# Optimization experiments

Hardware: AMD Instinct MI355X
Metric: run time of the kernel (lower is better)

Reference implementation:

```python
import jax, jax.numpy as jnp
import numpy as np

N = 131072      # num nodes
T = 16          # tile (block) size, tile_rows == tile_cols
BR = N // T     # block rows = 8192
K = 8           # nonzero blocks per block-row
IN_F, HID, NCLS = 128, 256, 64
LN_EPS = 1e-5


def setup_inputs() -> dict:
    key = jax.random.key(0)
    ks = jax.random.split(key, 8)
    features = jax.random.normal(ks[0], (N, IN_F), dtype=jnp.float32)
    block_vals = jax.random.uniform(ks[1], (BR, K, T, T), dtype=jnp.float32) / (K * T)
    block_cols = jax.random.randint(ks[2], (BR, K), 0, BR, dtype=jnp.int32)
    W0 = jax.random.normal(ks[3], (IN_F, HID), dtype=jnp.float32) / np.sqrt(IN_F)
    W1 = jax.random.normal(ks[4], (HID, HID), dtype=jnp.float32) / np.sqrt(HID)
    W2 = jax.random.normal(ks[5], (HID, NCLS), dtype=jnp.float32) / np.sqrt(HID)
    return {
        "features": features,
        "block_vals": block_vals,
        "W0": W0, "b0": jnp.zeros((HID,), jnp.float32),
        "W1": W1, "b1": jnp.zeros((HID,), jnp.float32),
        "W2": W2, "b2": jnp.zeros((NCLS,), jnp.float32),
        "g0": jnp.ones((HID,), jnp.float32), "beta0": jnp.zeros((HID,), jnp.float32),
        "g1": jnp.ones((HID,), jnp.float32), "beta1": jnp.zeros((HID,), jnp.float32),
        "block_cols": block_cols,
    }


def bcsr_spmm(block_vals, block_cols, z):
    """Block-CSR sparse matmul: out = A @ z.
    block_vals: [BR, K, T, T], block_cols: [BR, K] (block-column ids), z: [N, F]."""
    f = z.shape[-1]
    zb = z.reshape(BR, T, f)[block_cols]          # gather column blocks -> [BR, K, T, F]
    out = jnp.einsum('bkrc,bkcf->brf', block_vals, zb)  # block GEMM + accumulate over K
    return out.reshape(N, f)


def layer_norm(x, g, b):
    mu = jnp.mean(x, axis=-1, keepdims=True)
    var = jnp.mean(jnp.square(x - mu), axis=-1, keepdims=True)
    return g * (x - mu) * jax.lax.rsqrt(var + LN_EPS) + b


def reference(features, block_vals, W0, b0, W1, b1, W2, b2,
              g0, beta0, g1, beta1, block_cols):
    # layer 0: h' = A @ (h W0) + b0 ; relu ; LayerNorm
    h = bcsr_spmm(block_vals, block_cols, features @ W0) + b0
    h = layer_norm(jax.nn.relu(h), g0, beta0)
    # layer 1
    h = bcsr_spmm(block_vals, block_cols, h @ W1) + b1
    h = layer_norm(jax.nn.relu(h), g1, beta1)
    # output layer (no activation/norm)
    h = bcsr_spmm(block_vals, block_cols, h @ W2) + b2
    return h
```

## Files before the change

### kernel.cpp

```cpp
#include <hip/hip_runtime.h>
#include <hip/hip_bf16.h>


typedef __bf16 bf16;
typedef bf16 bf16x8 __attribute__((ext_vector_type(8)));
typedef bf16 bf16x4 __attribute__((ext_vector_type(4)));
typedef float f32x4 __attribute__((ext_vector_type(4)));

#define N_NODES 131072
#define BRQ 8192
#define KNZ 8
#define IN_F 128
#define HID 256
#define NCLS 64

static __device__ __forceinline__ f32x4 mfma16(bf16x8 a, bf16x8 b, f32x4 c) {
  return __builtin_amdgcn_mfma_f32_16x16x32_bf16(a, b, c, 0, 0, 0);
}

static __device__ __forceinline__ bf16x8 load8(const bf16* p) {
  return *(const bf16x8*)p;
}
static __device__ __forceinline__ bf16x8 load8(const float* p) {
  f32x4 a0 = *(const f32x4*)p;
  f32x4 a1 = *(const f32x4*)(p + 4);
  bf16x8 r;
  r[0] = (bf16)a0[0]; r[1] = (bf16)a0[1]; r[2] = (bf16)a0[2]; r[3] = (bf16)a0[3];
  r[4] = (bf16)a1[0]; r[5] = (bf16)a1[1]; r[6] = (bf16)a1[2]; r[7] = (bf16)a1[3];
  return r;
}

__global__ void transpose_cvt(const float* __restrict__ in, bf16* __restrict__ out,
                              int rows, int cols) {
  int idx = blockIdx.x * 256 + threadIdx.x;
  if (idx < rows * cols) {
    int r = idx / cols, c = idx - r * cols;
    out[c * rows + r] = (bf16)in[idx];
  }
}

template<typename TA, int KIN, int FOUT, int GRID>
__global__ __launch_bounds__(256) void gemm_bt(const TA* __restrict__ X,
                                               const bf16* __restrict__ WT,
                                               bf16* __restrict__ Zbt) {
  constexpr int CG  = FOUT / 64;
  constexpr int KS  = KIN / 32;
  constexpr int RTS = GRID * 4 / CG;
  constexpr int NT  = BRQ / RTS;

  const int wave = threadIdx.x >> 6;
  const int lane = threadIdx.x & 63;
  const int l15  = lane & 15;
  const int quad = lane >> 4;
  const int gw   = blockIdx.x * 4 + wave;
  const int cg   = gw % CG;
  const int rt0  = gw / CG;

  const bf16* __restrict__ wbase = WT + (long)(cg * 64 + l15) * KIN + quad * 8;
  bf16x8 bfr[KS][4];
#pragma unroll
  for (int k = 0; k < KS; ++k)
#pragma unroll
    for (int t = 0; t < 4; ++t)
      bfr[k][t] = *(const bf16x8*)(wbase + t * (16 * KIN) + k * 32);

  const TA* __restrict__ xbase = X + (long)l15 * KIN + quad * 8;

  bf16x8 aw[2][KS];
#pragma unroll
  for (int k = 0; k < KS; ++k)
    aw[0][k] = load8(xbase + (long)rt0 * (16 * KIN) + k * 32);

#pragma unroll
  for (int it = 0; it < NT; ++it) {
    const int rt = rt0 + it * RTS;
    if (it + 1 < NT) {
      const long xoff = (long)(rt + RTS) * (16 * KIN);
#pragma unroll
      for (int k = 0; k < KS; ++k)
        aw[(it + 1) & 1][k] = load8(xbase + xoff + k * 32);
    }
    f32x4 acc[4] = {};
#pragma unroll
    for (int k = 0; k < KS; ++k)
#pragma unroll
      for (int t = 0; t < 4; ++t)
        acc[t] = mfma16(aw[it & 1][k], bfr[k][t], acc[t]);
#pragma unroll
    for (int t = 0; t < 4; ++t) {
      int col = cg * 64 + t * 16 + l15;
      bf16x4 v;
#pragma unroll
      for (int i = 0; i < 4; ++i) v[i] = (bf16)acc[t][i];
      *(bf16x4*)(Zbt + ((long)rt * FOUT + col) * 16 + quad * 4) = v;
    }
  }
}

__global__ __launch_bounds__(256) void spmm_ln(const float* __restrict__ Abv,
                                               const int*   __restrict__ Abc,
                                               const bf16*  __restrict__ Zbt,
                                               const float* __restrict__ bias,
                                               const float* __restrict__ gamma,
                                               const float* __restrict__ beta,
                                               bf16* __restrict__ H) {
  const int b    = blockIdx.x;
  const int wave = threadIdx.x >> 6;
  const int lane = threadIdx.x & 63;
  const int l15  = lane & 15;
  const int quad = lane >> 4;

  const int*   bc    = Abc + b * KNZ;
  const int    cst   = (quad & 1) * 8;
  const int    half  = quad >> 1;
  const float* abase = Abv + (long)b * (KNZ * 256) + l15 * 16 + cst;

  bf16x8 afr[4];
  long   zb[4];
#pragma unroll
  for (int kp = 0; kp < 4; ++kp) {
    int blk = 2 * kp + half;
    afr[kp] = load8(abase + blk * 256);
    zb[kp]  = (long)bc[blk] * (HID * 16) + cst;
  }
  bf16x8 bfr[4][4];
#pragma unroll
  for (int kp = 0; kp < 4; ++kp)
#pragma unroll
    for (int t = 0; t < 4; ++t) {
      int f = wave * 64 + t * 16 + l15;
      bfr[kp][t] = *(const bf16x8*)(Zbt + zb[kp] + f * 16);
    }

  f32x4 acc[4] = {};
#pragma unroll
  for (int kp = 0; kp < 4; ++kp)
#pragma unroll
    for (int t = 0; t < 4; ++t)
      acc[t] = mfma16(afr[kp], bfr[kp][t], acc[t]);

  __shared__ float ld[16][257];
#pragma unroll
  for (int t = 0; t < 4; ++t) {
    int f = wave * 64 + t * 16 + l15;
    float bi = bias[f];
#pragma unroll
    for (int i = 0; i < 4; ++i) {
      float v = acc[t][i] + bi;
      ld[quad * 4 + i][f] = v > 0.f ? v : 0.f;
    }
  }
  __syncthreads();

#pragma unroll
  for (int rr = 0; rr < 4; ++rr) {
    int r = wave * 4 + rr;
    float v0 = ld[r][lane], v1 = ld[r][64 + lane];
    float v2 = ld[r][128 + lane], v3 = ld[r][192 + lane];
    float s  = v0 + v1 + v2 + v3;
    float ss = v0 * v0 + v1 * v1 + v2 * v2 + v3 * v3;
#pragma unroll
    for (int m = 1; m < 64; m <<= 1) {
      s  += __shfl_xor(s, m, 64);
      ss += __shfl_xor(ss, m, 64);
    }
    float mu   = s * (1.f / 256.f);
    float var  = ss * (1.f / 256.f) - mu * mu;
    float rstd = rsqrtf(var + 1e-5f);
    bf16* hrow = H + (long)(b * 16 + r) * HID;
    float vv[4] = {v0, v1, v2, v3};
#pragma unroll
    for (int k2 = 0; k2 < 4; ++k2) {
      int f = k2 * 64 + lane;
      float y = (vv[k2] - mu) * rstd * gamma[f] + beta[f];
      hrow[f] = (bf16)y;
    }
  }
}

__global__ __launch_bounds__(256) void spmm_out(const float* __restrict__ Abv,
                                                const int*   __restrict__ Abc,
                                                const bf16*  __restrict__ Zbt,
                                                const float* __restrict__ bias,
                                                float* __restrict__ out) {
  const int wave = threadIdx.x >> 6;
  const int b    = blockIdx.x * 4 + wave;
  const int lane = threadIdx.x & 63;
  const int l15  = lane & 15;
  const int quad = lane >> 4;

  const int*   bc    = Abc + b * KNZ;
  const int    cst   = (quad & 1) * 8;
  const int    half  = quad >> 1;
  const float* abase = Abv + (long)b * (KNZ * 256) + l15 * 16 + cst;

  bf16x8 afr[4];
  long   zb[4];
#pragma unroll
  for (int kp = 0; kp < 4; ++kp) {
    int blk = 2 * kp + half;
    afr[kp] = load8(abase + blk * 256);
    zb[kp]  = (long)bc[blk] * (NCLS * 16) + cst;
  }
  bf16x8 bfr[4][4];
#pragma unroll
  for (int kp = 0; kp < 4; ++kp)
#pragma unroll
    for (int t = 0; t < 4; ++t) {
      int f = t * 16 + l15;
      bfr[kp][t] = *(const bf16x8*)(Zbt + zb[kp] + f * 16);
    }

  f32x4 acc[4] = {};
#pragma unroll
  for (int kp = 0; kp < 4; ++kp)
#pragma unroll
    for (int t = 0; t < 4; ++t)
      acc[t] = mfma16(afr[kp], bfr[kp][t], acc[t]);

#pragma unroll
  for (int t = 0; t < 4; ++t) {
    int f = t * 16 + l15;
    float bi = bias[f];
#pragma unroll
    for (int i = 0; i < 4; ++i) {
      out[(long)(b * 16 + quad * 4 + i) * NCLS + f] = acc[t][i] + bi;
    }
  }
}

extern "C" void kernel_launch(void* const* d_in, const int* in_sizes, int n_in,
                              void* d_out, int out_size, void* d_ws, size_t ws_size,
                              hipStream_t stream) {
  const float* features = (const float*)d_in[0];
  const float* bvals    = (const float*)d_in[1];
  const float* W0       = (const float*)d_in[2];
  const float* b0       = (const float*)d_in[3];
  const float* W1       = (const float*)d_in[4];
  const float* b1       = (const float*)d_in[5];
  const float* W2       = (const float*)d_in[6];
  const float* b2       = (const float*)d_in[7];
  const float* g0       = (const float*)d_in[8];
  const float* beta0    = (const float*)d_in[9];
  const float* g1       = (const float*)d_in[10];
  const float* beta1    = (const float*)d_in[11];
  const int*   bcols    = (const int*)d_in[12];
  float* outp = (float*)d_out;

  bf16* zbt = (bf16*)d_ws;
  bf16* h   = zbt + (size_t)N_NODES * HID;

  bf16* w0t = (bf16*)d_out;
  bf16* w1t = w0t + IN_F * HID;
  bf16* w2t = w1t + HID * HID;

  transpose_cvt<<<dim3((IN_F * HID + 255) / 256), dim3(256), 0, stream>>>(W0, w0t, IN_F, HID);
  transpose_cvt<<<dim3((HID * HID + 255) / 256), dim3(256), 0, stream>>>(W1, w1t, HID, HID);
  transpose_cvt<<<dim3((HID * NCLS + 255) / 256), dim3(256), 0, stream>>>(W2, w2t, HID, NCLS);

  gemm_bt<float, IN_F, HID, 1024><<<dim3(1024), dim3(256), 0, stream>>>(features, w0t, zbt);
  spmm_ln<<<dim3(BRQ), dim3(256), 0, stream>>>(bvals, bcols, zbt, b0, g0, beta0, h);
  gemm_bt<bf16, HID, HID, 1024><<<dim3(1024), dim3(256), 0, stream>>>(h, w1t, zbt);
  spmm_ln<<<dim3(BRQ), dim3(256), 0, stream>>>(bvals, bcols, zbt, b1, g1, beta1, h);
  gemm_bt<bf16, HID, NCLS, 512><<<dim3(512), dim3(256), 0, stream>>>(h, w2t, zbt);
  spmm_out<<<dim3(BRQ / 4), dim3(256), 0, stream>>>(bvals, bcols, zbt, b2, outp);
}
```

Measured before the change: 466.1 us.

## Process two block-rows per workgroup in spmm_ln with register LayerNorm reduction

spmm_ln now assigns each block-row to a pair of waves, each covering 128 features, so one workgroup handles two block-rows. The LayerNorm statistics are reduced in registers with shuffles plus a small shared-memory exchange between the wave pair, replacing the 16x257 float shared-memory staging of the whole tile. The three weight transpose launches are merged into one kernel. Each wave now holds twice as many B fragments and accumulators, which raises register pressure and may lower occupancy, and the per-lane row stores are scattered 2-byte writes.

```diff
diff --git a/kernel.cpp b/kernel.cpp
--- a/kernel.cpp
+++ b/kernel.cpp
@@ -30,12 +30,19 @@
   return r;
 }
 
-__global__ void transpose_cvt(const float* __restrict__ in, bf16* __restrict__ out,
-                              int rows, int cols) {
+__global__ void transpose_all(const float* __restrict__ W0, const float* __restrict__ W1,
+                              const float* __restrict__ W2, bf16* __restrict__ w0t,
+                              bf16* __restrict__ w1t, bf16* __restrict__ w2t) {
   int idx = blockIdx.x * 256 + threadIdx.x;
-  if (idx < rows * cols) {
-    int r = idx / cols, c = idx - r * cols;
-    out[c * rows + r] = (bf16)in[idx];
+  if (idx < 32768) {
+    int r = idx >> 8, c = idx & 255;
+    w0t[c * 128 + r] = (bf16)W0[idx];
+  } else if (idx < 98304) {
+    int j = idx - 32768; int r = j >> 8, c = j & 255;
+    w1t[c * 256 + r] = (bf16)W1[j];
+  } else {
+    int j = idx - 98304; int r = j >> 6, c = j & 63;
+    w2t[c * 256 + r] = (bf16)W2[j];
   }
 }
 
@@ -104,11 +111,12 @@
                                                const float* __restrict__ gamma,
                                                const float* __restrict__ beta,
                                                bf16* __restrict__ H) {
-  const int b    = blockIdx.x;
   const int wave = threadIdx.x >> 6;
   const int lane = threadIdx.x & 63;
   const int l15  = lane & 15;
   const int quad = lane >> 4;
+  const int b    = blockIdx.x * 2 + (wave >> 1);
+  const int ch   = wave & 1;
 
   const int*   bc    = Abc + b * KNZ;
   const int    cst   = (quad & 1) * 8;
@@ -123,56 +131,72 @@
     afr[kp] = load8(abase + blk * 256);
     zb[kp]  = (long)bc[blk] * (HID * 16) + cst;
   }
-  bf16x8 bfr[4][4];
-#pragma unroll
-  for (int kp = 0; kp < 4; ++kp)
-#pragma unroll
-    for (int t = 0; t < 4; ++t) {
-      int f = wave * 64 + t * 16 + l15;
+  bf16x8 bfr[4][8];
+#pragma unroll
+  for (int kp = 0; kp < 4; ++kp)
+#pragma unroll
+    for (int t = 0; t < 8; ++t) {
+      int f = ch * 128 + t * 16 + l15;
       bfr[kp][t] = *(const bf16x8*)(Zbt + zb[kp] + f * 16);
     }
 
-  f32x4 acc[4] = {};
-#pragma unroll
-  for (int kp = 0; kp < 4; ++kp)
-#pragma unroll
-    for (int t = 0; t < 4; ++t)
+  f32x4 acc[8] = {};
+#pragma unroll
+  for (int kp = 0; kp < 4; ++kp)
+#pragma unroll
+    for (int t = 0; t < 8; ++t)
       acc[t] = mfma16(afr[kp], bfr[kp][t], acc[t]);
 
-  __shared__ float ld[16][257];
-#pragma unroll
-  for (int t = 0; t < 4; ++t) {
-    int f = wave * 64 + t * 16 + l15;
-    float bi = bias[f];
+  float gv[8], bv[8];
+#pragma unroll
+  for (int t = 0; t < 8; ++t) {
+    int f = ch * 128 + t * 16 + l15;
+    gv[t] = gamma[f];
+    bv[t] = beta[f];
+  }
+  float ps[4] = {0.f, 0.f, 0.f, 0.f}, pss[4] = {0.f, 0.f, 0.f, 0.f};
+#pragma unroll
+  for (int t = 0; t < 8; ++t) {
+    float bi = bias[ch * 128 + t * 16 + l15];
 #pragma unroll
     for (int i = 0; i < 4; ++i) {
       float v = acc[t][i] + bi;
-      ld[quad * 4 + i][f] = v > 0.f ? v : 0.f;
+      v = v > 0.f ? v : 0.f;
+      acc[t][i] = v;
+      ps[i] += v;
+      pss[i] += v * v;
+    }
+  }
+#pragma unroll
+  for (int m = 1; m < 16; m <<= 1) {
+#pragma unroll
+    for (int i = 0; i < 4; ++i) {
+      ps[i]  += __shfl_xor(ps[i], m, 64);
+      pss[i] += __shfl_xor(pss[i], m, 64);
+    }
+  }
+  __shared__ float S[4][16], SS[4][16];
+  if (l15 == 0) {
+#pragma unroll
+    for (int i = 0; i < 4; ++i) {
+      S[wave][quad * 4 + i]  = ps[i];
+      SS[wave][quad * 4 + i] = pss[i];
     }
   }
   __syncthreads();
-
-#pragma unroll
-  for (int rr = 0; rr < 4; ++rr) {
-    int r = wave * 4 + rr;
-    float v0 = ld[r][lane], v1 = ld[r][64 + lane];
-    float v2 = ld[r][128 + lane], v3 = ld[r][192 + lane];
-    float s  = v0 + v1 + v2 + v3;
-    float ss = v0 * v0 + v1 * v1 + v2 * v2 + v3 * v3;
-#pragma unroll
-    for (int m = 1; m < 64; m <<= 1) {
-      s  += __shfl_xor(s, m, 64);
-      ss += __shfl_xor(ss, m, 64);
-    }
+#pragma unroll
+  for (int i = 0; i < 4; ++i) {
+    int r = quad * 4 + i;
+    float s    = S[wave][r] + S[wave ^ 1][r];
+    float ss   = SS[wave][r] + SS[wave ^ 1][r];
     float mu   = s * (1.f / 256.f);
     float var  = ss * (1.f / 256.f) - mu * mu;
     float rstd = rsqrtf(var + 1e-5f);
     bf16* hrow = H + (long)(b * 16 + r) * HID;
-    float vv[4] = {v0, v1, v2, v3};
-#pragma unroll
-    for (int k2 = 0; k2 < 4; ++k2) {
-      int f = k2 * 64 + lane;
-      float y = (vv[k2] - mu) * rstd * gamma[f] + beta[f];
+#pragma unroll
+    for (int t = 0; t < 8; ++t) {
+      int f = ch * 128 + t * 16 + l15;
+      float y = (acc[t][i] - mu) * rstd * gv[t] + bv[t];
       hrow[f] = (bf16)y;
     }
   }
@@ -254,14 +278,12 @@
   bf16* w1t = w0t + IN_F * HID;
   bf16* w2t = w1t + HID * HID;
 
-  transpose_cvt<<<dim3((IN_F * HID + 255) / 256), dim3(256), 0, stream>>>(W0, w0t, IN_F, HID);
-  transpose_cvt<<<dim3((HID * HID + 255) / 256), dim3(256), 0, stream>>>(W1, w1t, HID, HID);
-  transpose_cvt<<<dim3((HID * NCLS + 255) / 256), dim3(256), 0, stream>>>(W2, w2t, HID, NCLS);
+  transpose_all<<<dim3(448), dim3(256), 0, stream>>>(W0, W1, W2, w0t, w1t, w2t);
 
   gemm_bt<float, IN_F, HID, 1024><<<dim3(1024), dim3(256), 0, stream>>>(features, w0t, zbt);
-  spmm_ln<<<dim3(BRQ), dim3(256), 0, stream>>>(bvals, bcols, zbt, b0, g0, beta0, h);
+  spmm_ln<<<dim3(BRQ / 2), dim3(256), 0, stream>>>(bvals, bcols, zbt, b0, g0, beta0, h);
   gemm_bt<bf16, HID, HID, 1024><<<dim3(1024), dim3(256), 0, stream>>>(h, w1t, zbt);
-  spmm_ln<<<dim3(BRQ), dim3(256), 0, stream>>>(bvals, bcols, zbt, b1, g1, beta1, h);
+  spmm_ln<<<dim3(BRQ / 2), dim3(256), 0, stream>>>(bvals, bcols, zbt, b1, g1, beta1, h);
   gemm_bt<bf16, HID, NCLS, 512><<<dim3(512), dim3(256), 0, stream>>>(h, w2t, zbt);
   spmm_out<<<dim3(BRQ / 4), dim3(256), 0, stream>>>(bvals, bcols, zbt, b2, outp);
 }
```

Measured after the change: 464.5 us. No clear change (-0.3%).
